# Optimization experiments

Measured on AMD Instinct MI355X. Metric: run time of the kernel, lower is better.

The kernel has to match this reference:

```python
import jax, jax.numpy as jnp
import numpy as np

L = 6        # gnn_layers
H = 4        # heads
C = 128      # per-head channels = hidden // heads
HID = 512    # hidden
IN = 768     # in_dim
N = 20000    # nodes
E = 320000   # edges
P = 100000   # scored pairs


def _gelu(v):
    return jax.nn.gelu(v, approximate=False)


def _ln(v, g, b):
    m = v.mean(-1, keepdims=True)
    var = v.var(-1, keepdims=True)
    return (v - m) / jnp.sqrt(var + 1e-5) * g + b


def setup_inputs() -> dict:
    key = jax.random.key(0)
    ks = jax.random.split(key, 24)
    g = lambda k, shape, s=0.02: (jax.random.normal(k, shape, jnp.float32) * s)
    inp = {}
    inp["x"] = jax.random.normal(ks[0], (N, IN), jnp.float32)
    inp["edge_index"] = jax.random.randint(ks[1], (2, E), 0, N)
    inp["edges"] = jax.random.randint(ks[2], (2, P), 0, N)
    # FeatureMixer (no alt branch)
    inp["mixer_W"] = g(ks[3], (IN, HID)); inp["mixer_b"] = jnp.zeros((HID,), jnp.float32)
    # Stacked TransformerConv params per layer
    inp["Wq"] = g(ks[4], (L, HID, HID)); inp["bq"] = jnp.zeros((L, HID), jnp.float32)
    inp["Wk"] = g(ks[5], (L, HID, HID)); inp["bk"] = jnp.zeros((L, HID), jnp.float32)
    inp["Wv"] = g(ks[6], (L, HID, HID)); inp["bv"] = jnp.zeros((L, HID), jnp.float32)
    inp["Ws"] = g(ks[7], (L, HID, HID)); inp["bs"] = jnp.zeros((L, HID), jnp.float32)  # lin_skip (root weight)
    inp["ln_g"] = jnp.ones((L, HID), jnp.float32); inp["ln_b"] = jnp.zeros((L, HID), jnp.float32)
    # Dual projections
    inp["syn_W"] = g(ks[8], (HID, HID)); inp["syn_b"] = jnp.zeros((HID,), jnp.float32)
    inp["ant_W"] = g(ks[9], (HID, HID)); inp["ant_b"] = jnp.zeros((HID,), jnp.float32)
    # Bilinear score matrices
    inp["W_syn"] = g(ks[10], (HID, HID), 0.04)
    inp["W_ant"] = g(ks[11], (HID, HID), 0.04)
    # Gate MLP: Linear(4*HID, HID) -> GELU -> Linear(HID, 1) -> Sigmoid
    inp["gW1"] = g(ks[12], (4 * HID, HID)); inp["gb1"] = jnp.zeros((HID,), jnp.float32)
    inp["gW2"] = g(ks[13], (HID, 1)); inp["gb2"] = jnp.zeros((1,), jnp.float32)
    return inp


def reference(x, edge_index, edges, mixer_W, mixer_b, Wq, bq, Wk, bk, Wv, bv,
              Ws, bs, ln_g, ln_b, syn_W, syn_b, ant_W, ant_b, W_syn, W_ant,
              gW1, gb1, gW2, gb2):
    src, dst = edge_index[0], edge_index[1]
    scale = 1.0 / np.sqrt(C).astype(np.float32)
    # FeatureMixer (eval mode: dropout = identity)
    h = _gelu(x @ mixer_W + mixer_b)  # [N, HID]
    for l in range(L):
        # node-side projections, then gather per edge
        q = (h @ Wq[l] + bq[l]).reshape(N, H, C)
        k = (h @ Wk[l] + bk[l]).reshape(N, H, C)
        v = (h @ Wv[l] + bv[l]).reshape(N, H, C)
        logits = (q[dst] * k[src]).sum(-1) * scale          # [E, H]
        mx = jax.ops.segment_max(logits, dst, num_segments=N)   # [N, H]
        ex = jnp.exp(logits - mx[dst])
        den = jax.ops.segment_sum(ex, dst, num_segments=N)      # [N, H]
        alpha = ex / den[dst]                                   # segment softmax over incoming edges
        msg = alpha[..., None] * v[src]                         # [E, H, C]
        out = jax.ops.segment_sum(msg, dst, num_segments=N).reshape(N, HID)
        out = out + h @ Ws[l] + bs[l]                           # root/skip term of TransformerConv
        out = _gelu(out)
        h = _ln(h + out, ln_g[l], ln_b[l])
    z_syn = _gelu(h @ syn_W + syn_b)
    z_ant = _gelu(h @ ant_W + ant_b)
    i, j = edges[0], edges[1]
    vi_s, vj_s = z_syn[i], z_syn[j]
    vi_a, vj_a = z_ant[i], z_ant[j]
    s_syn = ((vi_s @ W_syn) * vj_s).sum(-1)
    s_ant = ((vi_a @ W_ant) * vj_a).sum(-1)
    pair = jnp.concatenate([jnp.abs(vi_s - vj_s), vi_s * vj_s,
                            jnp.abs(vi_a - vj_a), vi_a * vj_a], axis=-1)  # [P, 4*HID]
    g = jax.nn.sigmoid(_gelu(pair @ gW1 + gb1) @ gW2 + gb2).squeeze(-1)
    return g * s_ant + (1.0 - g) * (-s_syn)
```

## Files before the change

### kernel.cpp

```cpp
#include <hip/hip_runtime.h>
#include <cstdint>

#define L_LAYERS 6

typedef __attribute__((ext_vector_type(8))) short bf16x8;
typedef __attribute__((ext_vector_type(4))) float f32x4;
typedef __attribute__((ext_vector_type(2))) float f32x2;

__device__ __forceinline__ float gelu1(float v) {
    return 0.5f * v * (1.0f + erff(v * 0.7071067811865475f));
}

__device__ __forceinline__ unsigned int f2bf2(float a, float b) {
    union { float f; unsigned u; } x, y;
    x.f = a; y.f = b;
    unsigned lo = (x.u + 0x7FFFu + ((x.u >> 16) & 1u)) >> 16;
    unsigned hi = (y.u + 0x7FFFu + ((y.u >> 16) & 1u)) & 0xFFFF0000u;
    return lo | hi;
}

__device__ __forceinline__ unsigned short f2bf1(float a) {
    union { float f; unsigned u; } x;
    x.f = a;
    return (unsigned short)((x.u + 0x7FFFu + ((x.u >> 16) & 1u)) >> 16);
}

__device__ __forceinline__ unsigned cvt_pk_bf16(float lo, float hi) {
    unsigned r;
    asm("v_cvt_pk_bf16_f32 %0, %1, %2" : "=v"(r) : "v"(lo), "v"(hi));
    return r;
}

__device__ __forceinline__ float2 bfp2(unsigned u) {
    union { unsigned u; float f; } a, b;
    a.u = u << 16;
    b.u = u & 0xFFFF0000u;
    return make_float2(a.f, b.f);
}

__device__ __forceinline__ void gload16(const void* g, void* l) {
    __builtin_amdgcn_global_load_lds(
        (const __attribute__((address_space(1))) void*)g,
        (__attribute__((address_space(3))) void*)l, 16, 0, 0);
}


__global__ void k_zero(int* __restrict__ p, int n) {
    int i = blockIdx.x * 256 + threadIdx.x;
    if (i < n) p[i] = 0;
}


__global__ void k_hist(const int* __restrict__ dst, int* __restrict__ hist, int E) {
    int e = blockIdx.x * 256 + threadIdx.x;
    if (e < E) atomicAdd(&hist[dst[e]], 1);
}

__global__ __launch_bounds__(1024) void k_scan(const int* __restrict__ hist,
                                               int* __restrict__ off, int n) {
    __shared__ int buf[1024];
    __shared__ int carry;
    int tid = threadIdx.x;
    if (tid == 0) carry = 0;
    __syncthreads();
    for (int base = 0; base < n; base += 1024) {
        int v = (base + tid < n) ? hist[base + tid] : 0;
        buf[tid] = v;
        __syncthreads();
        int x = v;
        for (int o = 1; o < 1024; o <<= 1) {
            int t = (tid >= o) ? buf[tid - o] : 0;
            __syncthreads();
            x += t;
            buf[tid] = x;
            __syncthreads();
        }
        int c = carry;
        if (base + tid < n) off[base + tid] = c + x - v;
        __syncthreads();
        if (tid == 1023) carry = c + buf[1023];
        __syncthreads();
    }
    if (tid == 0) off[n] = carry;
}

__global__ void k_scatter(const int* __restrict__ src, const int* __restrict__ dst,
                          const int* __restrict__ off, int* __restrict__ cursor,
                          int* __restrict__ srcS, int E) {
    int e = blockIdx.x * 256 + threadIdx.x;
    if (e < E) {
        int d = dst[e];
        int pos = off[d] + atomicAdd(&cursor[d], 1);
        srcS[pos] = src[e];
    }
}


__global__ void k_wcat(const float* __restrict__ Wq, const float* __restrict__ Wk,
                       const float* __restrict__ Wv, const float* __restrict__ Ws,
                       short* __restrict__ Wt) {
    int idx = blockIdx.x * 256 + threadIdx.x;
    int k = idx & 511;
    int nf = (idx >> 9) & 2047;
    int l = idx >> 20;
    int sel = nf >> 9, nn = nf & 511;
    const float* W = (sel == 0) ? Wq : (sel == 1) ? Wk : (sel == 2) ? Wv : Ws;
    float v = W[((size_t)l * 512 + k) * 512 + nn];
    Wt[idx] = (short)f2bf1(v);
}

__global__ void k_tr(const float* __restrict__ W, short* __restrict__ Wt, int K, int N,
                     int swz) {
    int k = blockIdx.x * 256 + threadIdx.x;
    int n = blockIdx.y;
    if (k < K) {
        int kk = k;
        if (swz) kk = (k & ~31) | (((((k >> 3) & 3) ^ ((n >> 1) & 3))) << 3) | (k & 7);
        Wt[(size_t)n * K + kk] = (short)f2bf1(W[(size_t)k * N + n]);
    }
}

__global__ void k_bcat(const float* __restrict__ bq, const float* __restrict__ bk,
                       const float* __restrict__ bv, const float* __restrict__ bs,
                       float* __restrict__ bcat) {
    int idx = blockIdx.x * 256 + threadIdx.x;
    if (idx >= L_LAYERS * 2048) return;
    int l = idx >> 11, n = idx & 2047;
    int sel = n >> 9, nn = n & 511;
    const float* b = (sel == 0) ? bq : (sel == 1) ? bk : (sel == 2) ? bv : bs;
    bcat[idx] = b[l * 512 + nn];
}

__global__ void k_bdual(const float* __restrict__ sb, const float* __restrict__ ab,
                        float* __restrict__ bd) {
    int idx = blockIdx.x * 256 + threadIdx.x;
    if (idx < 1024) bd[idx] = (idx < 512) ? sb[idx] : ab[idx - 512];
}


__global__ __launch_bounds__(256) void gemm_a32(
    const float* __restrict__ A, int lda,
    const short* __restrict__ Bt,
    const float* __restrict__ bias,
    float* __restrict__ Cf, short* __restrict__ Cbf, int ldc,
    int M, int N, int K, int act) {
    __shared__ __align__(16) short As[128][40];
    __shared__ __align__(16) short Bs[128][40];
    const int tid = threadIdx.x;
    const int lane = tid & 63;
    const int wave = tid >> 6;
    const int wr = (wave >> 1) * 64;
    const int wc = (wave & 1) * 64;
    const int l16 = lane & 15;
    const int quad = lane >> 4;
    const int row0 = blockIdx.x * 128;
    const int col0 = blockIdx.y * 128;
    const int sr = tid >> 2;
    const int sk = (tid & 3) * 8;

    f32x4 acc[4][4];
#pragma unroll
    for (int i = 0; i < 4; ++i)
#pragma unroll
        for (int j = 0; j < 4; ++j)
            acc[i][j] = f32x4{0.f, 0.f, 0.f, 0.f};

    for (int kb = 0; kb < K; kb += 32) {
#pragma unroll
        for (int hh = 0; hh < 2; ++hh) {
            int r = sr + hh * 64;
            int gr = row0 + r;
            float4 a0, a1;
            if (gr < M) {
                const float* p = A + (size_t)gr * lda + kb + sk;
                a0 = *(const float4*)p;
                a1 = *(const float4*)(p + 4);
            } else {
                a0 = make_float4(0.f, 0.f, 0.f, 0.f);
                a1 = make_float4(0.f, 0.f, 0.f, 0.f);
            }
            uint4 av;
            av.x = f2bf2(a0.x, a0.y);
            av.y = f2bf2(a0.z, a0.w);
            av.z = f2bf2(a1.x, a1.y);
            av.w = f2bf2(a1.z, a1.w);
            *(uint4*)&As[r][sk] = av;
            const short* bp = Bt + (size_t)(col0 + r) * K + kb + sk;
            *(uint4*)&Bs[r][sk] = *(const uint4*)bp;
        }
        __syncthreads();
        bf16x8 af[4], bfr[4];
#pragma unroll
        for (int i = 0; i < 4; ++i)
            af[i] = *(const bf16x8*)&As[wr + i * 16 + l16][quad * 8];
#pragma unroll
        for (int j = 0; j < 4; ++j)
            bfr[j] = *(const bf16x8*)&Bs[wc + j * 16 + l16][quad * 8];
#pragma unroll
        for (int i = 0; i < 4; ++i)
#pragma unroll
            for (int j = 0; j < 4; ++j)
                acc[i][j] = __builtin_amdgcn_mfma_f32_16x16x32_bf16(af[i], bfr[j], acc[i][j], 0, 0, 0);
        __syncthreads();
    }
#pragma unroll
    for (int i = 0; i < 4; ++i) {
        int rbase = row0 + wr + i * 16 + quad * 4;
#pragma unroll
        for (int j = 0; j < 4; ++j) {
            int c = col0 + wc + j * 16 + l16;
            float bv = bias ? bias[c] : 0.0f;
#pragma unroll
            for (int rg = 0; rg < 4; ++rg) {
                int gr = rbase + rg;
                if (gr < M) {
                    float v = acc[i][j][rg] + bv;
                    if (act) v = gelu1(v);
                    Cf[(size_t)gr * ldc + c] = v;
                    if (Cbf) Cbf[(size_t)gr * ldc + c] = (short)f2bf1(v);
                }
            }
        }
    }
}


__global__ __launch_bounds__(256) void gemm_bb(
    const short* __restrict__ A, int lda,
    const short* __restrict__ Bt,
    const float* __restrict__ bias,
    short* __restrict__ C, unsigned char* __restrict__ C8, int ldc,
    int M, int N, int K, int act) {
    __shared__ __align__(16) short As[128 * 32];
    __shared__ __align__(16) short Bs[128 * 32];
    const int tid = threadIdx.x;
    const int lane = tid & 63;
    const int wave = tid >> 6;
    const int wr = (wave >> 1) * 64;
    const int wc = (wave & 1) * 64;
    const int l16 = lane & 15;
    const int quad = lane >> 4;
    const int row0 = blockIdx.x * 128;
    const int col0 = blockIdx.y * 128;
    const int c0 = tid, c1 = tid + 256;
    const int r0 = c0 >> 2, kq0 = (c0 & 3) * 8;
    const int r1 = c1 >> 2, kq1 = (c1 & 3) * 8;
    int ga0 = row0 + r0; if (ga0 >= M) ga0 = M - 1;
    int ga1 = row0 + r1; if (ga1 >= M) ga1 = M - 1;
    const short* Ap0 = A + (size_t)ga0 * lda + kq0;
    const short* Ap1 = A + (size_t)ga1 * lda + kq1;
    const short* Bp0 = Bt + (size_t)(col0 + r0) * K + kq0;
    const short* Bp1 = Bt + (size_t)(col0 + r1) * K + kq1;

    f32x4 acc[4][4];
#pragma unroll
    for (int i = 0; i < 4; ++i)
#pragma unroll
        for (int j = 0; j < 4; ++j)
            acc[i][j] = f32x4{0.f, 0.f, 0.f, 0.f};

    for (int kb = 0; kb < K; kb += 32) {
        gload16(Ap0 + kb, &As[c0 * 8]);
        gload16(Ap1 + kb, &As[c1 * 8]);
        gload16(Bp0 + kb, &Bs[c0 * 8]);
        gload16(Bp1 + kb, &Bs[c1 * 8]);
        __syncthreads();
        bf16x8 af[4], bfr[4];
#pragma unroll
        for (int i = 0; i < 4; ++i)
            af[i] = *(const bf16x8*)&As[(wr + i * 16 + l16) * 32 + quad * 8];
#pragma unroll
        for (int j = 0; j < 4; ++j)
            bfr[j] = *(const bf16x8*)&Bs[(wc + j * 16 + l16) * 32 + quad * 8];
#pragma unroll
        for (int i = 0; i < 4; ++i)
#pragma unroll
            for (int j = 0; j < 4; ++j)
                acc[i][j] = __builtin_amdgcn_mfma_f32_16x16x32_bf16(af[i], bfr[j], acc[i][j], 0, 0, 0);
        __syncthreads();
    }
#pragma unroll
    for (int i = 0; i < 4; ++i) {
        int rbase = row0 + wr + i * 16 + quad * 4;
#pragma unroll
        for (int j = 0; j < 4; ++j) {
            int c = col0 + wc + j * 16 + l16;
            float bv = bias ? bias[c] : 0.0f;
#pragma unroll
            for (int rg = 0; rg < 4; ++rg) {
                int gr = rbase + rg;
                if (gr < M) {
                    float v = acc[i][j][rg] + bv;
                    if (act) v = gelu1(v);
                    C[(size_t)gr * ldc + c] = (short)f2bf1(v);
                    if (C8) {
                        int r8 = __builtin_amdgcn_cvt_pk_fp8_f32(v, v, 0, false);
                        C8[(size_t)gr * ldc + c] = (unsigned char)(r8 & 0xFF);
                    }
                }
            }
        }
    }
}


__global__ __launch_bounds__(256) void gemm_qkvs(
    const short* __restrict__ A,
    const short* __restrict__ Bt,
    const float* __restrict__ bias,
    short* __restrict__ qvs,
    unsigned char* __restrict__ kv8,
    int M, int mtiles) {
    const int K = 512;
    const int id = blockIdx.x;
    const int xcd = id & 7;
    const int t = id >> 3;
    const int col_t = t & 15;
    const int row_t = (t >> 4) * 8 + xcd;
    if (row_t >= mtiles) return;
    const int row0 = row_t * 128;
    const int col0 = col_t * 128;
    __shared__ __align__(16) short As[128 * 32];
    __shared__ __align__(16) short Bs[128 * 32];
    const int tid = threadIdx.x;
    const int lane = tid & 63;
    const int wave = tid >> 6;
    const int wr = (wave >> 1) * 64;
    const int wc = (wave & 1) * 64;
    const int l16 = lane & 15;
    const int quad = lane >> 4;
    const int c0 = tid, c1 = tid + 256;
    const int r0 = c0 >> 2, kq0 = (c0 & 3) * 8;
    const int r1 = c1 >> 2, kq1 = (c1 & 3) * 8;
    int ga0 = row0 + r0; if (ga0 >= M) ga0 = M - 1;
    int ga1 = row0 + r1; if (ga1 >= M) ga1 = M - 1;
    const short* Ap0 = A + (size_t)ga0 * K + kq0;
    const short* Ap1 = A + (size_t)ga1 * K + kq1;
    const short* Bp0 = Bt + (size_t)(col0 + r0) * K + kq0;
    const short* Bp1 = Bt + (size_t)(col0 + r1) * K + kq1;

    f32x4 acc[4][4];
#pragma unroll
    for (int i = 0; i < 4; ++i)
#pragma unroll
        for (int j = 0; j < 4; ++j)
            acc[i][j] = f32x4{0.f, 0.f, 0.f, 0.f};

    for (int kb = 0; kb < K; kb += 32) {
        gload16(Ap0 + kb, &As[c0 * 8]);
        gload16(Ap1 + kb, &As[c1 * 8]);
        gload16(Bp0 + kb, &Bs[c0 * 8]);
        gload16(Bp1 + kb, &Bs[c1 * 8]);
        __syncthreads();
        bf16x8 af[4], bfr[4];
#pragma unroll
        for (int i = 0; i < 4; ++i)
            af[i] = *(const bf16x8*)&As[(wr + i * 16 + l16) * 32 + quad * 8];
#pragma unroll
        for (int j = 0; j < 4; ++j)
            bfr[j] = *(const bf16x8*)&Bs[(wc + j * 16 + l16) * 32 + quad * 8];
#pragma unroll
        for (int i = 0; i < 4; ++i)
#pragma unroll
            for (int j = 0; j < 4; ++j)
                acc[i][j] = __builtin_amdgcn_mfma_f32_16x16x32_bf16(af[i], bfr[j], acc[i][j], 0, 0, 0);
        __syncthreads();
    }
#pragma unroll
    for (int i = 0; i < 4; ++i) {
        int rbase = row0 + wr + i * 16 + quad * 4;
#pragma unroll
        for (int j = 0; j < 4; ++j) {
            int c = col0 + wc + j * 16 + l16;
            int sec = c >> 9;
            int cc = c & 511;
            float bv = bias[c];
#pragma unroll
            for (int rg = 0; rg < 4; ++rg) {
                int gr = rbase + rg;
                if (gr < M) {
                    float v = acc[i][j][rg] + bv;
                    if (sec == 1 || sec == 2) {
                        int r8 = __builtin_amdgcn_cvt_pk_fp8_f32(v, v, 0, false);
                        int off = (sec == 1) ? cc : 512 + cc;
                        kv8[(size_t)gr * 1024 + off] = (unsigned char)(r8 & 0xFF);
                    } else {
                        int off = (sec == 0) ? cc : 512 + cc;
                        qvs[(size_t)gr * 1024 + off] = (short)f2bf1(v);
                    }
                }
            }
        }
    }
}


__global__ __launch_bounds__(512, 2) void gemm_gate(
    const unsigned char* __restrict__ z8,
    const int* __restrict__ pi, const int* __restrict__ pj, int P,
    const short* __restrict__ Bt,
    const float* __restrict__ gb1,
    const float* __restrict__ gW2,
    float* __restrict__ gpart) {
    __shared__ __align__(16) short Bab[2 * 512 * 32];
    __shared__ __align__(16) short Bmu[2 * 512 * 32];
    __shared__ __align__(16) short Asab[128 * 32];
    __shared__ __align__(16) short Asmu[128 * 32];
    __shared__ int iArr[128];
    __shared__ int jArr[128];
    __shared__ float rowsum[128];
    const int row0 = blockIdx.x * 128;
    const int tid = threadIdx.x;
    const int lane = tid & 63;
    const int wave = tid >> 6;
    const int wm = wave >> 2;
    const int wn = wave & 3;
    const int l16 = lane & 15;
    const int quad = lane >> 4;
    const int arow = tid >> 2;
    const int aslot = tid & 3;
    const int qs = (quad ^ ((l16 >> 1) & 3)) * 8;
    const int awoff = arow * 32 + ((aslot ^ ((arow >> 1) & 3)) << 3);

    if (tid < 128) {
        int p = row0 + tid;
        int ok = (p < P);
        iArr[tid] = ok ? pi[p] : 0;
        jArr[tid] = ok ? pj[p] : 0;
        rowsum[tid] = 0.0f;
    }
    __syncthreads();
    const unsigned char* zi = z8 + (size_t)iArr[arow] * 1024 + aslot * 8;
    const unsigned char* zj = z8 + (size_t)jArr[arow] * 1024 + aslot * 8;
    const short* brow = Bt + (size_t)(tid >> 2) * 2048 + (tid & 3) * 8;

    f32x4 acc[4][8];
#pragma unroll
    for (int i = 0; i < 4; ++i)
#pragma unroll
        for (int j = 0; j < 8; ++j)
            acc[i][j] = f32x4{0.f, 0.f, 0.f, 0.f};

    auto CHB = [](int kc) { return ((kc >> 4) << 10) + ((kc & 15) << 5); };
    auto KOFF = [](int kc) { return ((kc >> 4) << 9) + ((kc & 15) << 5); };
    auto STAGE = [&](int kc, int mu, short* buf) {
        const short* src = brow + CHB(kc) + (mu ? 512 : 0);
#pragma unroll
        for (int g = 0; g < 4; ++g)
            gload16(src + (size_t)(g * 128) * 2048, buf + (g * 512 + tid) * 8);
    };
    auto CVT = [&](uint2 xu, uint2 yu, uint4& aa, uint4& am) {
        f32x2 x0 = __builtin_amdgcn_cvt_pk_f32_fp8((int)xu.x, false);
        f32x2 x1 = __builtin_amdgcn_cvt_pk_f32_fp8((int)xu.x, true);
        f32x2 x2 = __builtin_amdgcn_cvt_pk_f32_fp8((int)xu.y, false);
        f32x2 x3 = __builtin_amdgcn_cvt_pk_f32_fp8((int)xu.y, true);
        f32x2 y0 = __builtin_amdgcn_cvt_pk_f32_fp8((int)yu.x, false);
        f32x2 y1 = __builtin_amdgcn_cvt_pk_f32_fp8((int)yu.x, true);
        f32x2 y2 = __builtin_amdgcn_cvt_pk_f32_fp8((int)yu.y, false);
        f32x2 y3 = __builtin_amdgcn_cvt_pk_f32_fp8((int)yu.y, true);
        aa.x = cvt_pk_bf16(fabsf(x0.x - y0.x), fabsf(x0.y - y0.y));
        aa.y = cvt_pk_bf16(fabsf(x1.x - y1.x), fabsf(x1.y - y1.y));
        aa.z = cvt_pk_bf16(fabsf(x2.x - y2.x), fabsf(x2.y - y2.y));
        aa.w = cvt_pk_bf16(fabsf(x3.x - y3.x), fabsf(x3.y - y3.y));
        am.x = cvt_pk_bf16(x0.x * y0.x, x0.y * y0.y);
        am.y = cvt_pk_bf16(x1.x * y1.x, x1.y * y1.y);
        am.z = cvt_pk_bf16(x2.x * y2.x, x2.y * y2.y);
        am.w = cvt_pk_bf16(x3.x * y3.x, x3.y * y3.y);
    };
    auto MFMA_PHASE = [&](const short* As, const short* Bp) {
        bf16x8 af[4];
#pragma unroll
        for (int i = 0; i < 4; ++i)
            af[i] = *(const bf16x8*)&As[(wm * 64 + i * 16 + l16) * 32 + qs];
#pragma unroll
        for (int j = 0; j < 8; ++j) {
            bf16x8 bf = *(const bf16x8*)&Bp[(wn * 128 + j * 16 + l16) * 32 + qs];
#pragma unroll
            for (int i = 0; i < 4; ++i)
                acc[i][j] = __builtin_amdgcn_mfma_f32_16x16x32_bf16(af[i], bf, acc[i][j], 0, 0, 0);
        }
    };

    STAGE(0, 0, Bab);
    uint2 xu = *(const uint2*)zi;
    uint2 yu = *(const uint2*)zj;
    uint4 aa, am, am_hold;
    CVT(xu, yu, aa, am);
    *(uint4*)&Asab[awoff] = aa;
    am_hold = am;

#pragma unroll 1
    for (int kc = 0; kc < 31; ++kc) {
        const int cur = kc & 1;
        STAGE(kc, 1, Bmu + cur * 16384);
        uint2 xn = *(const uint2*)(zi + KOFF(kc + 1));
        uint2 yn = *(const uint2*)(zj + KOFF(kc + 1));
        asm volatile("s_waitcnt vmcnt(6) lgkmcnt(0)" ::: "memory");
        __builtin_amdgcn_s_barrier();
        MFMA_PHASE(Asab, Bab + cur * 16384);
        *(uint4*)&Asmu[awoff] = am_hold;
        STAGE(kc + 1, 0, Bab + (cur ^ 1) * 16384);
        CVT(xn, yn, aa, am);
        asm volatile("s_waitcnt vmcnt(4) lgkmcnt(0)" ::: "memory");
        __builtin_amdgcn_s_barrier();
        MFMA_PHASE(Asmu, Bmu + cur * 16384);
        *(uint4*)&Asab[awoff] = aa;
        am_hold = am;
    }
    STAGE(31, 1, Bmu + 16384);
    asm volatile("s_waitcnt vmcnt(4) lgkmcnt(0)" ::: "memory");
    __builtin_amdgcn_s_barrier();
    MFMA_PHASE(Asab, Bab + 16384);
    *(uint4*)&Asmu[awoff] = am_hold;
    asm volatile("s_waitcnt vmcnt(0) lgkmcnt(0)" ::: "memory");
    __builtin_amdgcn_s_barrier();
    MFMA_PHASE(Asmu, Bmu + 16384);

#pragma unroll
    for (int i = 0; i < 4; ++i) {
#pragma unroll
        for (int rg = 0; rg < 4; ++rg) {
            float partial = 0.f;
#pragma unroll
            for (int j = 0; j < 8; ++j) {
                int cc = wn * 128 + j * 16 + l16;
                partial += gelu1(acc[i][j][rg] + gb1[cc]) * gW2[cc];
            }
            partial += __shfl_xor(partial, 1);
            partial += __shfl_xor(partial, 2);
            partial += __shfl_xor(partial, 4);
            partial += __shfl_xor(partial, 8);
            if (l16 == 0)
                atomicAdd(&rowsum[wm * 64 + i * 16 + quad * 4 + rg], partial);
        }
    }
    __syncthreads();
    if (tid < 128) {
        int p = row0 + tid;
        if (p < P) gpart[p] = rowsum[tid];
    }
}


__global__ __launch_bounds__(256) void k_attn(const short* __restrict__ qvs,
                                              const unsigned char* __restrict__ kv8,
                                              const int* __restrict__ srcS,
                                              const int* __restrict__ offs,
                                              float* __restrict__ h,
                                              short* __restrict__ h_bf,
                                              const float* __restrict__ lng,
                                              const float* __restrict__ lnb, int Nn) {
    const int tid = threadIdx.x;
    const int lane = tid & 63;
    const int wv = tid >> 6;
    const int n = blockIdx.x * 4 + wv;
    if (n >= Nn) return;
    const int st = offs[n], en = offs[n + 1];
    const size_t chOff = (size_t)lane * 8;

    uint4 qv = *(const uint4*)(qvs + (size_t)n * 1024 + chOff);
    float2 q0 = bfp2(qv.x), q1 = bfp2(qv.y), q2 = bfp2(qv.z), q3 = bfp2(qv.w);
    float acc[8];
#pragma unroll
    for (int i = 0; i < 8; ++i) acc[i] = 0.f;
    float m_l = -3.4e38f, l_l = 0.f;

    auto PROC = [&](uint2 kq, uint2 vq) {
        f32x2 k0 = __builtin_amdgcn_cvt_pk_f32_fp8((int)kq.x, false);
        f32x2 k1 = __builtin_amdgcn_cvt_pk_f32_fp8((int)kq.x, true);
        f32x2 k2 = __builtin_amdgcn_cvt_pk_f32_fp8((int)kq.y, false);
        f32x2 k3 = __builtin_amdgcn_cvt_pk_f32_fp8((int)kq.y, true);
        float d = q0.x * k0.x + q0.y * k0.y + q1.x * k1.x + q1.y * k1.y +
                  q2.x * k2.x + q2.y * k2.y + q3.x * k3.x + q3.y * k3.y;
        d += __shfl_xor(d, 1);
        d += __shfl_xor(d, 2);
        d += __shfl_xor(d, 4);
        d += __shfl_xor(d, 8);
        float lg = d * 0.08838834764831845f;
        float m_new = fmaxf(m_l, lg);
        float sc = __expf(m_l - m_new);
        float p = __expf(lg - m_new);
        l_l = l_l * sc + p;
        m_l = m_new;
        f32x2 v0 = __builtin_amdgcn_cvt_pk_f32_fp8((int)vq.x, false);
        f32x2 v1 = __builtin_amdgcn_cvt_pk_f32_fp8((int)vq.x, true);
        f32x2 v2 = __builtin_amdgcn_cvt_pk_f32_fp8((int)vq.y, false);
        f32x2 v3 = __builtin_amdgcn_cvt_pk_f32_fp8((int)vq.y, true);
        acc[0] = acc[0] * sc + p * v0.x; acc[1] = acc[1] * sc + p * v0.y;
        acc[2] = acc[2] * sc + p * v1.x; acc[3] = acc[3] * sc + p * v1.y;
        acc[4] = acc[4] * sc + p * v2.x; acc[5] = acc[5] * sc + p * v2.y;
        acc[6] = acc[6] * sc + p * v3.x; acc[7] = acc[7] * sc + p * v3.y;
    };

    for (int e0 = st; e0 < en; e0 += 64) {
        int cnt = min(64, en - e0);
        int myS = (lane < cnt) ? srcS[e0 + lane] : 0;
        int ei = 0;
        for (; ei + 4 <= cnt; ei += 4) {
            int s0 = __shfl(myS, ei);
            int s1 = __shfl(myS, ei + 1);
            int s2 = __shfl(myS, ei + 2);
            int s3 = __shfl(myS, ei + 3);
            const unsigned char* r0 = kv8 + (size_t)s0 * 1024 + chOff;
            const unsigned char* r1 = kv8 + (size_t)s1 * 1024 + chOff;
            const unsigned char* r2 = kv8 + (size_t)s2 * 1024 + chOff;
            const unsigned char* r3 = kv8 + (size_t)s3 * 1024 + chOff;
            uint2 ka = *(const uint2*)r0;
            uint2 va = *(const uint2*)(r0 + 512);
            uint2 kb = *(const uint2*)r1;
            uint2 vb = *(const uint2*)(r1 + 512);
            uint2 kc = *(const uint2*)r2;
            uint2 vc = *(const uint2*)(r2 + 512);
            uint2 kd = *(const uint2*)r3;
            uint2 vd = *(const uint2*)(r3 + 512);
            PROC(ka, va);
            PROC(kb, vb);
            PROC(kc, vc);
            PROC(kd, vd);
        }
        for (; ei < cnt; ++ei) {
            int s = __shfl(myS, ei);
            const unsigned char* srow = kv8 + (size_t)s * 1024 + chOff;
            uint2 kq = *(const uint2*)srow;
            uint2 vq = *(const uint2*)(srow + 512);
            PROC(kq, vq);
        }
    }
    float rinv = (en > st) ? 1.0f / l_l : 0.f;
    uint4 su = *(const uint4*)(qvs + (size_t)n * 1024 + 512 + chOff);
    float2 s0 = bfp2(su.x), s1 = bfp2(su.y), s2 = bfp2(su.z), s3 = bfp2(su.w);
    float sv[8] = {s0.x, s0.y, s1.x, s1.y, s2.x, s2.y, s3.x, s3.y};
    const float* hp = h + (size_t)n * 512 + chOff;
    float4 h0 = *(const float4*)hp;
    float4 h1 = *(const float4*)(hp + 4);
    float hv[8] = {h0.x, h0.y, h0.z, h0.w, h1.x, h1.y, h1.z, h1.w};
    float r[8];
    float sum = 0.f, ssq = 0.f;
#pragma unroll
    for (int i = 0; i < 8; ++i) {
        r[i] = hv[i] + gelu1(acc[i] * rinv + sv[i]);
        sum += r[i];
        ssq += r[i] * r[i];
    }
    for (int o = 32; o; o >>= 1) {
        sum += __shfl_xor(sum, o);
        ssq += __shfl_xor(ssq, o);
    }
    float mean = sum * (1.0f / 512.0f);
    float var = ssq * (1.0f / 512.0f) - mean * mean;
    float inv = rsqrtf(var + 1e-5f);
    const float* gp = lng + chOff;
    const float* bp = lnb + chOff;
    float4 g0 = *(const float4*)gp, g1 = *(const float4*)(gp + 4);
    float4 b0 = *(const float4*)bp, b1 = *(const float4*)(bp + 4);
    float ga[8] = {g0.x, g0.y, g0.z, g0.w, g1.x, g1.y, g1.z, g1.w};
    float ba[8] = {b0.x, b0.y, b0.z, b0.w, b1.x, b1.y, b1.z, b1.w};
    float o8[8];
#pragma unroll
    for (int i = 0; i < 8; ++i) o8[i] = (r[i] - mean) * inv * ga[i] + ba[i];
    float* hw = h + (size_t)n * 512 + chOff;
    *(float4*)hw = make_float4(o8[0], o8[1], o8[2], o8[3]);
    *(float4*)(hw + 4) = make_float4(o8[4], o8[5], o8[6], o8[7]);
    uint4 ob;
    ob.x = f2bf2(o8[0], o8[1]);
    ob.y = f2bf2(o8[2], o8[3]);
    ob.z = f2bf2(o8[4], o8[5]);
    ob.w = f2bf2(o8[6], o8[7]);
    *(uint4*)(h_bf + (size_t)n * 512 + chOff) = ob;
}


__global__ __launch_bounds__(256) void k_pairscore(const short* __restrict__ z,
                                                   const short* __restrict__ t,
                                                   const int* __restrict__ pi,
                                                   const int* __restrict__ pj,
                                                   float* __restrict__ ssyn,
                                                   float* __restrict__ sant, int P) {
    int p = blockIdx.x * 4 + (threadIdx.x >> 6);
    if (p >= P) return;
    int lane = threadIdx.x & 63;
    int i = pi[p], j = pj[p];
    uint4 a = *(const uint4*)(t + (size_t)i * 1024 + lane * 8);
    uint4 b = *(const uint4*)(z + (size_t)j * 1024 + lane * 8);
    float2 a0 = bfp2(a.x), a1 = bfp2(a.y), a2 = bfp2(a.z), a3 = bfp2(a.w);
    float2 b0 = bfp2(b.x), b1 = bfp2(b.y), b2 = bfp2(b.z), b3 = bfp2(b.w);
    float ds = a0.x * b0.x + a0.y * b0.y + a1.x * b1.x + a1.y * b1.y +
               a2.x * b2.x + a2.y * b2.y + a3.x * b3.x + a3.y * b3.y;
    uint4 c = *(const uint4*)(t + (size_t)i * 1024 + 512 + lane * 8);
    uint4 d = *(const uint4*)(z + (size_t)j * 1024 + 512 + lane * 8);
    float2 c0 = bfp2(c.x), c1 = bfp2(c.y), c2 = bfp2(c.z), c3 = bfp2(c.w);
    float2 d0 = bfp2(d.x), d1 = bfp2(d.y), d2 = bfp2(d.z), d3 = bfp2(d.w);
    float da = c0.x * d0.x + c0.y * d0.y + c1.x * d1.x + c1.y * d1.y +
               c2.x * d2.x + c2.y * d2.y + c3.x * d3.x + c3.y * d3.y;
    for (int o = 32; o; o >>= 1) {
        ds += __shfl_xor(ds, o);
        da += __shfl_xor(da, o);
    }
    if (lane == 0) { ssyn[p] = ds; sant[p] = da; }
}


__global__ void k_final(const float* __restrict__ gpart, const float* __restrict__ gb2,
                        const float* __restrict__ ssyn, const float* __restrict__ sant,
                        float* __restrict__ out, int P) {
    int p = blockIdx.x * 256 + threadIdx.x;
    if (p < P) {
        float s = 1.0f / (1.0f + __expf(-(gpart[p] + gb2[0])));
        out[p] = s * sant[p] - (1.0f - s) * ssyn[p];
    }
}


extern "C" void kernel_launch(void* const* d_in, const int* in_sizes, int n_in,
                              void* d_out, int out_size, void* d_ws, size_t ws_size,
                              hipStream_t stream) {
    const float* x = (const float*)d_in[0];
    const int* ei = (const int*)d_in[1];
    const int* pe = (const int*)d_in[2];
    const float* mixer_W = (const float*)d_in[3];
    const float* mixer_b = (const float*)d_in[4];
    const float* Wq = (const float*)d_in[5];
    const float* bq = (const float*)d_in[6];
    const float* Wk = (const float*)d_in[7];
    const float* bk = (const float*)d_in[8];
    const float* Wv = (const float*)d_in[9];
    const float* bv = (const float*)d_in[10];
    const float* Ws = (const float*)d_in[11];
    const float* bs = (const float*)d_in[12];
    const float* ln_g = (const float*)d_in[13];
    const float* ln_b = (const float*)d_in[14];
    const float* syn_W = (const float*)d_in[15];
    const float* syn_b = (const float*)d_in[16];
    const float* ant_W = (const float*)d_in[17];
    const float* ant_b = (const float*)d_in[18];
    const float* W_syn = (const float*)d_in[19];
    const float* W_ant = (const float*)d_in[20];
    const float* gW1 = (const float*)d_in[21];
    const float* gb1 = (const float*)d_in[22];
    const float* gW2 = (const float*)d_in[23];
    const float* gb2 = (const float*)d_in[24];
    float* out = (float*)d_out;

    const int Nn = in_sizes[0] / 768;
    const int E = in_sizes[1] / 2;
    const int P = in_sizes[2] / 2;

    char* w = (char*)d_ws;
    auto alloc = [&](size_t bytes) -> char* {
        char* p = w;
        w += (bytes + 255) & ~(size_t)255;
        return p;
    };
    float* h = (float*)alloc((size_t)Nn * 512 * 4);
    short* h_bf = (short*)alloc((size_t)Nn * 512 * 2);
    char* U = alloc((size_t)Nn * 2048 * 2);
    short* qvs = (short*)U;
    unsigned char* kv8 = (unsigned char*)(U + (size_t)Nn * 1024 * 2);
    short* zB = (short*)U;
    short* tB = (short*)(U + (size_t)Nn * 1024 * 2);
    unsigned char* z8 = (unsigned char*)alloc((size_t)Nn * 1024);
    float* ssyn = (float*)alloc((size_t)P * 3 * 4);
    float* sant = ssyn + P;
    float* gpart = ssyn + 2 * P;
    int* srcS = (int*)alloc((size_t)E * 4);
    int* hist = (int*)alloc((size_t)Nn * 2 * 4);
    int* cursor = hist + Nn;
    int* offs = (int*)alloc((size_t)(Nn + 1) * 4);
    short* mixWt = (short*)alloc((size_t)512 * 768 * 2);
    short* wcat = (short*)alloc((size_t)L_LAYERS * 2048 * 512 * 2);
    short* dualWt = (short*)alloc((size_t)1024 * 512 * 2);
    short* bilWt = (short*)alloc((size_t)1024 * 512 * 2);
    short* gw1t = (short*)alloc((size_t)512 * 2048 * 2);
    float* bcat = (float*)alloc((size_t)L_LAYERS * 2048 * 4);
    float* bdual = (float*)alloc((size_t)1024 * 4);

    k_zero<<<(2 * Nn + 255) / 256, 256, 0, stream>>>(hist, 2 * Nn);
    k_hist<<<(E + 255) / 256, 256, 0, stream>>>(ei + E, hist, E);
    k_scan<<<1, 1024, 0, stream>>>(hist, offs, Nn);
    k_scatter<<<(E + 255) / 256, 256, 0, stream>>>(ei, ei + E, offs, cursor, srcS, E);

    k_wcat<<<(L_LAYERS * 2048 * 512) / 256, 256, 0, stream>>>(Wq, Wk, Wv, Ws, wcat);
    k_tr<<<dim3(3, 512), 256, 0, stream>>>(mixer_W, mixWt, 768, 512, 0);
    k_tr<<<dim3(2, 512), 256, 0, stream>>>(syn_W, dualWt, 512, 512, 0);
    k_tr<<<dim3(2, 512), 256, 0, stream>>>(ant_W, dualWt + 512 * 512, 512, 512, 0);
    k_tr<<<dim3(2, 512), 256, 0, stream>>>(W_syn, bilWt, 512, 512, 0);
    k_tr<<<dim3(2, 512), 256, 0, stream>>>(W_ant, bilWt + 512 * 512, 512, 512, 0);
    k_tr<<<dim3(8, 512), 256, 0, stream>>>(gW1, gw1t, 2048, 512, 1);
    k_bcat<<<48, 256, 0, stream>>>(bq, bk, bv, bs, bcat);
    k_bdual<<<4, 256, 0, stream>>>(syn_b, ant_b, bdual);

    const int mtiles = (Nn + 127) / 128;
    gemm_a32<<<dim3(mtiles, 4), 256, 0, stream>>>(x, 768, mixWt, mixer_b, h, h_bf, 512,
                                                  Nn, 512, 768, 1);

    const int qk_grid = ((mtiles + 7) / 8) * 8 * 16;
    for (int l = 0; l < L_LAYERS; ++l) {
        gemm_qkvs<<<qk_grid, 256, 0, stream>>>(h_bf, wcat + (size_t)l * 2048 * 512,
                                               bcat + l * 2048, qvs, kv8, Nn, mtiles);
        k_attn<<<(Nn + 3) / 4, 256, 0, stream>>>(qvs, kv8, srcS, offs, h, h_bf,
                                                 ln_g + l * 512, ln_b + l * 512, Nn);
    }

    gemm_bb<<<dim3(mtiles, 8), 256, 0, stream>>>(h_bf, 512, dualWt, bdual, zB, z8, 1024,
                                                 Nn, 1024, 512, 1);
    gemm_bb<<<dim3(mtiles, 4), 256, 0, stream>>>(zB, 1024, bilWt, nullptr, tB, nullptr, 1024,
                                                 Nn, 512, 512, 0);
    gemm_bb<<<dim3(mtiles, 4), 256, 0, stream>>>(zB + 512, 1024, bilWt + 512 * 512, nullptr,
                                                 tB + 512, nullptr, 1024, Nn, 512, 512, 0);

    k_pairscore<<<(P + 3) / 4, 256, 0, stream>>>(zB, tB, pe, pe + P, ssyn, sant, P);

    const int ptiles2 = (P + 127) / 128;
    gemm_gate<<<ptiles2, 512, 0, stream>>>(z8, pe, pe + P, P, gw1t, gb1, gW2, gpart);
    k_final<<<(P + 255) / 256, 256, 0, stream>>>(gpart, gb2, ssyn, sant, out, P);
}
```

Baseline: 1.618 ms.

## Triple-buffer LDS tiles in bf16 GEMMs to overlap global loads with MFMA

Replaces the load-sync-compute-sync loop in gemm_bb and gemm_qkvs with a three-stage LDS ring buffer. Two k-tiles are prefetched up front, and each iteration waits only on the older loads with vmcnt(4) and a single barrier before issuing the next prefetch. This is meant to hide global-to-LDS latency behind the matrix multiplies and drop one barrier per k-step. In exchange it triples LDS use per block, which may lower occupancy, and it relies on exact vmcnt accounting of the gload16 instructions.

After: 1.617 ms. No clear change (-0.0%).

```diff
diff --git a/kernel.cpp b/kernel.cpp
--- a/kernel.cpp
+++ b/kernel.cpp
@@ -231,8 +231,8 @@
     const float* __restrict__ bias,
     short* __restrict__ C, unsigned char* __restrict__ C8, int ldc,
     int M, int N, int K, int act) {
-    __shared__ __align__(16) short As[128 * 32];
-    __shared__ __align__(16) short Bs[128 * 32];
+    __shared__ __align__(16) short As[3 * 128 * 32];
+    __shared__ __align__(16) short Bs[3 * 128 * 32];
     const int tid = threadIdx.x;
     const int lane = tid & 63;
     const int wave = tid >> 6;
@@ -259,25 +259,60 @@
         for (int j = 0; j < 4; ++j)
             acc[i][j] = f32x4{0.f, 0.f, 0.f, 0.f};
 
-    for (int kb = 0; kb < K; kb += 32) {
-        gload16(Ap0 + kb, &As[c0 * 8]);
-        gload16(Ap1 + kb, &As[c1 * 8]);
-        gload16(Bp0 + kb, &Bs[c0 * 8]);
-        gload16(Bp1 + kb, &Bs[c1 * 8]);
-        __syncthreads();
+    const int nsteps = K >> 5;
+    gload16(Ap0, &As[c0 * 8]);
+    gload16(Ap1, &As[c1 * 8]);
+    gload16(Bp0, &Bs[c0 * 8]);
+    gload16(Bp1, &Bs[c1 * 8]);
+    gload16(Ap0 + 32, &As[4096 + c0 * 8]);
+    gload16(Ap1 + 32, &As[4096 + c1 * 8]);
+    gload16(Bp0 + 32, &Bs[4096 + c0 * 8]);
+    gload16(Bp1 + 32, &Bs[4096 + c1 * 8]);
+    int cur = 0, nx2 = 2;
+#pragma unroll 1
+    for (int ks = 0; ks < nsteps - 1; ++ks) {
+        asm volatile("s_waitcnt vmcnt(4)" ::: "memory");
+        __builtin_amdgcn_s_barrier();
+        if (ks + 2 < nsteps) {
+            const int kb = (ks + 2) * 32;
+            const int nb = nx2 * 4096;
+            gload16(Ap0 + kb, &As[nb + c0 * 8]);
+            gload16(Ap1 + kb, &As[nb + c1 * 8]);
+            gload16(Bp0 + kb, &Bs[nb + c0 * 8]);
+            gload16(Bp1 + kb, &Bs[nb + c1 * 8]);
+        }
+        const int cb = cur * 4096;
         bf16x8 af[4], bfr[4];
 #pragma unroll
         for (int i = 0; i < 4; ++i)
-            af[i] = *(const bf16x8*)&As[(wr + i * 16 + l16) * 32 + quad * 8];
+            af[i] = *(const bf16x8*)&As[cb + (wr + i * 16 + l16) * 32 + quad * 8];
 #pragma unroll
         for (int j = 0; j < 4; ++j)
-            bfr[j] = *(const bf16x8*)&Bs[(wc + j * 16 + l16) * 32 + quad * 8];
+            bfr[j] = *(const bf16x8*)&Bs[cb + (wc + j * 16 + l16) * 32 + quad * 8];
 #pragma unroll
         for (int i = 0; i < 4; ++i)
 #pragma unroll
             for (int j = 0; j < 4; ++j)
                 acc[i][j] = __builtin_amdgcn_mfma_f32_16x16x32_bf16(af[i], bfr[j], acc[i][j], 0, 0, 0);
-        __syncthreads();
+        cur = (cur == 2) ? 0 : cur + 1;
+        nx2 = (nx2 == 2) ? 0 : nx2 + 1;
+    }
+    {
+        asm volatile("s_waitcnt vmcnt(0)" ::: "memory");
+        __builtin_amdgcn_s_barrier();
+        const int cb = cur * 4096;
+        bf16x8 af[4], bfr[4];
+#pragma unroll
+        for (int i = 0; i < 4; ++i)
+            af[i] = *(const bf16x8*)&As[cb + (wr + i * 16 + l16) * 32 + quad * 8];
+#pragma unroll
+        for (int j = 0; j < 4; ++j)
+            bfr[j] = *(const bf16x8*)&Bs[cb + (wc + j * 16 + l16) * 32 + quad * 8];
+#pragma unroll
+        for (int i = 0; i < 4; ++i)
+#pragma unroll
+            for (int j = 0; j < 4; ++j)
+                acc[i][j] = __builtin_amdgcn_mfma_f32_16x16x32_bf16(af[i], bfr[j], acc[i][j], 0, 0, 0);
     }
 #pragma unroll
     for (int i = 0; i < 4; ++i) {
@@ -320,8 +355,8 @@
     if (row_t >= mtiles) return;
     const int row0 = row_t * 128;
     const int col0 = col_t * 128;
-    __shared__ __align__(16) short As[128 * 32];
-    __shared__ __align__(16) short Bs[128 * 32];
+    __shared__ __align__(16) short As[3 * 128 * 32];
+    __shared__ __align__(16) short Bs[3 * 128 * 32];
     const int tid = threadIdx.x;
     const int lane = tid & 63;
     const int wave = tid >> 6;
@@ -346,25 +381,59 @@
         for (int j = 0; j < 4; ++j)
             acc[i][j] = f32x4{0.f, 0.f, 0.f, 0.f};
 
-    for (int kb = 0; kb < K; kb += 32) {
-        gload16(Ap0 + kb, &As[c0 * 8]);
-        gload16(Ap1 + kb, &As[c1 * 8]);
-        gload16(Bp0 + kb, &Bs[c0 * 8]);
-        gload16(Bp1 + kb, &Bs[c1 * 8]);
-        __syncthreads();
+    gload16(Ap0, &As[c0 * 8]);
+    gload16(Ap1, &As[c1 * 8]);
+    gload16(Bp0, &Bs[c0 * 8]);
+    gload16(Bp1, &Bs[c1 * 8]);
+    gload16(Ap0 + 32, &As[4096 + c0 * 8]);
+    gload16(Ap1 + 32, &As[4096 + c1 * 8]);
+    gload16(Bp0 + 32, &Bs[4096 + c0 * 8]);
+    gload16(Bp1 + 32, &Bs[4096 + c1 * 8]);
+    int cur = 0, nx2 = 2;
+#pragma unroll 1
+    for (int ks = 0; ks < 15; ++ks) {
+        asm volatile("s_waitcnt vmcnt(4)" ::: "memory");
+        __builtin_amdgcn_s_barrier();
+        if (ks + 2 < 16) {
+            const int kb = (ks + 2) * 32;
+            const int nb = nx2 * 4096;
+            gload16(Ap0 + kb, &As[nb + c0 * 8]);
+            gload16(Ap1 + kb, &As[nb + c1 * 8]);
+            gload16(Bp0 + kb, &Bs[nb + c0 * 8]);
+            gload16(Bp1 + kb, &Bs[nb + c1 * 8]);
+        }
+        const int cb = cur * 4096;
         bf16x8 af[4], bfr[4];
 #pragma unroll
         for (int i = 0; i < 4; ++i)
-            af[i] = *(const bf16x8*)&As[(wr + i * 16 + l16) * 32 + quad * 8];
+            af[i] = *(const bf16x8*)&As[cb + (wr + i * 16 + l16) * 32 + quad * 8];
 #pragma unroll
         for (int j = 0; j < 4; ++j)
-            bfr[j] = *(const bf16x8*)&Bs[(wc + j * 16 + l16) * 32 + quad * 8];
+            bfr[j] = *(const bf16x8*)&Bs[cb + (wc + j * 16 + l16) * 32 + quad * 8];
 #pragma unroll
         for (int i = 0; i < 4; ++i)
 #pragma unroll
             for (int j = 0; j < 4; ++j)
                 acc[i][j] = __builtin_amdgcn_mfma_f32_16x16x32_bf16(af[i], bfr[j], acc[i][j], 0, 0, 0);
-        __syncthreads();
+        cur = (cur == 2) ? 0 : cur + 1;
+        nx2 = (nx2 == 2) ? 0 : nx2 + 1;
+    }
+    {
+        asm volatile("s_waitcnt vmcnt(0)" ::: "memory");
+        __builtin_amdgcn_s_barrier();
+        const int cb = cur * 4096;
+        bf16x8 af[4], bfr[4];
+#pragma unroll
+        for (int i = 0; i < 4; ++i)
+            af[i] = *(const bf16x8*)&As[cb + (wr + i * 16 + l16) * 32 + quad * 8];
+#pragma unroll
+        for (int j = 0; j < 4; ++j)
+            bfr[j] = *(const bf16x8*)&Bs[cb + (wc + j * 16 + l16) * 32 + quad * 8];
+#pragma unroll
+        for (int i = 0; i < 4; ++i)
+#pragma unroll
+            for (int j = 0; j < 4; ++j)
+                acc[i][j] = __builtin_amdgcn_mfma_f32_16x16x32_bf16(af[i], bfr[j], acc[i][j], 0, 0, 0);
     }
 #pragma unroll
     for (int i = 0; i < 4; ++i) {
```
